# Kernel tuning notes

Measured on AMD Instinct MI355X. Metric: run time of the kernel, lower is better.

Reference implementation:

```python
import jax, jax.numpy as jnp
import numpy as np

B, T, D, NH, L = 8192, 100, 44, 64, 8  # batch, seq/ode steps, obs_dim, rnn hidden, latent


def setup_inputs() -> dict:
    key = jax.random.key(0)
    ks = jax.random.split(key, 12)
    s = 0.1
    return {
        "x": jax.random.normal(ks[0], (B, T, D), jnp.float32),
        "mask": jax.random.randint(ks[1], (B, T, D), 0, 2).astype(jnp.float32),
        "epsilon": jax.random.normal(ks[2], (B, L), jnp.float32),
        "Wi2h": jax.random.normal(ks[3], (D + NH, NH), jnp.float32) * s,
        "bi2h": jnp.zeros((NH,), jnp.float32),
        "Wh2o": jax.random.normal(ks[4], (NH, 2 * L), jnp.float32) * s,
        "bh2o": jnp.zeros((2 * L,), jnp.float32),
        "Wf1": jax.random.normal(ks[5], (L, NH), jnp.float32) * s,
        "bf1": jnp.zeros((NH,), jnp.float32),
        "Wf2": jax.random.normal(ks[6], (NH, NH), jnp.float32) * s,
        "bf2": jnp.zeros((NH,), jnp.float32),
        "Wf3": jax.random.normal(ks[7], (NH, L), jnp.float32) * s,
        "bf3": jnp.zeros((L,), jnp.float32),
        "Wd1": jax.random.normal(ks[8], (L, NH), jnp.float32) * s,
        "bd1": jnp.zeros((NH,), jnp.float32),
        "Wd2": jax.random.normal(ks[9], (NH, D), jnp.float32) * s,
        "bd2": jnp.zeros((D,), jnp.float32),
    }


def reference(x, mask, epsilon, Wi2h, bi2h, Wh2o, bh2o,
              Wf1, bf1, Wf2, bf2, Wf3, bf3, Wd1, bd1, Wd2, bd2):
    masked_x = x * mask  # [B,T,D]

    # --- reverse-time recognition RNN (scan over time, reversed) ---
    def rnn_step(h, obs):
        h = jnp.tanh(jnp.concatenate([obs, h], axis=1) @ Wi2h + bi2h)
        return h, None

    xs_rev = jnp.transpose(masked_x[:, ::-1, :], (1, 0, 2))  # [T,B,D]
    h0 = jnp.zeros((x.shape[0], Wi2h.shape[1]), x.dtype)
    h_final, _ = jax.lax.scan(rnn_step, h0, xs_rev)
    out = h_final @ Wh2o + bh2o  # [B,2L]
    qz0_mean, qz0_logvar = out[:, :L], out[:, L:]

    # reparameterized latent sample
    z0 = epsilon * jnp.exp(0.5 * qz0_logvar) + qz0_mean  # [B,L]

    # --- latent ODE dynamics, fixed-step RK4 over ts = linspace(0,1,100) ---
    def f(z):
        h1 = jax.nn.elu(z @ Wf1 + bf1)
        h2 = jax.nn.elu(h1 @ Wf2 + bf2)
        return h2 @ Wf3 + bf3

    dt = jnp.asarray(1.0 / (T - 1), x.dtype)

    def rk4_step(z, _):
        k1 = f(z)
        k2 = f(z + 0.5 * dt * k1)
        k3 = f(z + 0.5 * dt * k2)
        k4 = f(z + dt * k3)
        zn = z + (dt / 6.0) * (k1 + 2.0 * k2 + 2.0 * k3 + k4)
        return zn, zn

    _, zs = jax.lax.scan(rk4_step, z0, None, length=T - 1)  # [T-1,B,L]
    pred_z = jnp.transpose(jnp.concatenate([z0[None], zs], axis=0), (1, 0, 2))  # [B,T,L]

    # --- decoder ---
    pred_x = jax.nn.relu(pred_z @ Wd1 + bd1) @ Wd2 + bd2  # [B,T,D]

    # fill observed entries back in
    updated_x = jnp.where(masked_x != 0, masked_x, pred_x)

    # --- loss ---
    noise_logvar = 2.0 * jnp.log(jnp.asarray(0.3, x.dtype))
    log2pi = jnp.log(jnp.asarray(2.0 * np.pi, x.dtype))
    logpx = (-0.5 * (log2pi + noise_logvar +
                     (x - updated_x) ** 2 / jnp.exp(noise_logvar))).sum((-1, -2))  # [B]
    kl = (-0.5 * qz0_logvar + (jnp.exp(qz0_logvar) + qz0_mean ** 2) / 2.0 - 0.5).sum(-1)  # [B]
    loss = jnp.mean(-logpx + kl)
    return loss
```

## Files before the change

kernel.cpp:

```cpp
#include <hip/hip_runtime.h>
#include <stdint.h>


constexpr int B_ = 8192, T_ = 100, D_ = 44, NH_ = 64, L_ = 8;

typedef float f32x4 __attribute__((ext_vector_type(4)));
typedef uint32_t u32x2 __attribute__((ext_vector_type(2)));

#if __has_builtin(__builtin_amdgcn_mfma_f32_16x16x16bf16_1k)
typedef short frag16 __attribute__((ext_vector_type(4)));
#define MFMA16(a, b, c) __builtin_amdgcn_mfma_f32_16x16x16bf16_1k(a, b, c, 0, 0, 0)
#define USE_F16 0
#elif __has_builtin(__builtin_amdgcn_mfma_f32_16x16x16_bf16_1k)
typedef short frag16 __attribute__((ext_vector_type(4)));
#define MFMA16(a, b, c) __builtin_amdgcn_mfma_f32_16x16x16_bf16_1k(a, b, c, 0, 0, 0)
#define USE_F16 0
#elif __has_builtin(__builtin_amdgcn_mfma_f32_16x16x16_bf16)
typedef __bf16 frag16 __attribute__((ext_vector_type(4)));
#define MFMA16(a, b, c) __builtin_amdgcn_mfma_f32_16x16x16_bf16(a, b, c, 0, 0, 0)
#define USE_F16 0
#else
typedef _Float16 frag16 __attribute__((ext_vector_type(4)));
#define MFMA16(a, b, c) __builtin_amdgcn_mfma_f32_16x16x16f16(a, b, c, 0, 0, 0)
#define USE_F16 1
#endif

__device__ __forceinline__ float fexp2(float x) { return __builtin_amdgcn_exp2f(x); }
__device__ __forceinline__ float frcp(float x) { return __builtin_amdgcn_rcpf(x); }
__device__ __forceinline__ float fexp(float x) { return fexp2(x * 1.44269504088896341f); }
__device__ __forceinline__ float tanh_f(float x) {
  float e = fexp2(x * 2.88539008177792681f);
  return 1.0f - 2.0f * frcp(e + 1.0f);
}
__device__ __forceinline__ float elu_f(float x) { return x > 0.0f ? x : (fexp(x) - 1.0f); }

__device__ __forceinline__ uint32_t EW(float v) {
#if USE_F16
  return (uint32_t)__builtin_bit_cast(unsigned short, (_Float16)v);
#else
  return (uint32_t)__builtin_bit_cast(unsigned short, (__bf16)v);
#endif
}
__device__ __forceinline__ uint32_t PK2(float lo, float hi) { return EW(lo) | (EW(hi) << 16); }
__device__ __forceinline__ frag16 fr4(float a, float b, float c, float d) {
  u32x2 u = {PK2(a, b), PK2(c, d)};
  return __builtin_bit_cast(frag16, u);
}
__device__ __forceinline__ frag16 frpk(f32x4 v) {
  u32x2 u = {PK2(v[0], v[1]), PK2(v[2], v[3])};
  return __builtin_bit_cast(frag16, u);
}
__device__ __forceinline__ float f4get(const float4& f, int i) {
  return i == 0 ? f.x : (i == 1 ? f.y : (i == 2 ? f.z : f.w));
}

__global__ __launch_bounds__(64) void fused_kernel(
    const float* __restrict__ x, const float* __restrict__ mask,
    const float* __restrict__ eps,
    const float* __restrict__ Wi2h, const float* __restrict__ bi2h,
    const float* __restrict__ Wh2o, const float* __restrict__ bh2o,
    const float* __restrict__ Wf1, const float* __restrict__ bf1,
    const float* __restrict__ Wf2, const float* __restrict__ bf2,
    const float* __restrict__ Wf3, const float* __restrict__ bf3,
    const float* __restrict__ Wd1, const float* __restrict__ bd1,
    const float* __restrict__ Wd2, const float* __restrict__ bd2,
    float* __restrict__ part) {
  const int lane = threadIdx.x;
  const int c = lane & 15, q = lane >> 4;
  const int r0 = blockIdx.x * 16;
  const f32x4 fzero = {0.f, 0.f, 0.f, 0.f};
  const frag16 fgbias = fr4(1.0f, 0.f, 0.f, 0.f);

  frag16 Ai[4][7];
#pragma unroll
  for (int tau = 0; tau < 4; ++tau)
#pragma unroll
    for (int kc = 0; kc < 7; ++kc) {
      const int m = 16 * tau + c;
      float wv[4];
#pragma unroll
      for (int i = 0; i < 4; ++i) {
        const int k = 16 * kc + 4 * q + i;
        float v = 0.0f;
        if (k < 64) v = Wi2h[(44 + k) * 64 + m];
        else if (k < 108) v = Wi2h[(k - 64) * 64 + m];
        else if (k == 108) v = bi2h[m];
        wv[i] = v;
      }
      Ai[tau][kc] = fr4(wv[0], wv[1], wv[2], wv[3]);
    }
  frag16 Ah2o[4];
#pragma unroll
  for (int kc = 0; kc < 4; ++kc) {
    float wv[4];
#pragma unroll
    for (int i = 0; i < 4; ++i) wv[i] = Wh2o[(16 * kc + 4 * q + i) * 16 + c];
    Ah2o[kc] = fr4(wv[0], wv[1], wv[2], wv[3]);
  }
  f32x4 bo;
#pragma unroll
  for (int r = 0; r < 4; ++r) bo[r] = bh2o[4 * q + r];

  const float* xrowbase = x + (size_t)(r0 + c) * T_ * D_;
  const float* mrowbase = mask + (size_t)(r0 + c) * T_ * D_;

  auto load_obs = [&](int t, float4* xv, float4* mv) {
    const float* xp = xrowbase + (size_t)t * D_;
    const float* mp = mrowbase + (size_t)t * D_;
    xv[0] = *(const float4*)(xp + 4 * q);
    mv[0] = *(const float4*)(mp + 4 * q);
    xv[1] = *(const float4*)(xp + 16 + 4 * q);
    mv[1] = *(const float4*)(mp + 16 + 4 * q);
    float4 zz = {0.f, 0.f, 0.f, 0.f};
    xv[2] = zz; mv[2] = zz;
    if (q < 3) {
      xv[2] = *(const float4*)(xp + 32 + 4 * q);
      mv[2] = *(const float4*)(mp + 32 + 4 * q);
    }
  };

  f32x4 hc[4] = {};
  float4 xo[3], mo[3];
  load_obs(T_ - 1, xo, mo);

#pragma unroll 1
  for (int s = 0; s < T_; ++s) {
    const int t = T_ - 1 - s;
    float4 cx[3], cm[3];
#pragma unroll
    for (int j = 0; j < 3; ++j) { cx[j] = xo[j]; cm[j] = mo[j]; }
    if (t > 0) load_obs(t - 1, xo, mo);

    frag16 ob[3];
#pragma unroll
    for (int j = 0; j < 2; ++j) {
      u32x2 u = {PK2(cx[j].x * cm[j].x, cx[j].y * cm[j].y),
                 PK2(cx[j].z * cm[j].z, cx[j].w * cm[j].w)};
      ob[j] = __builtin_bit_cast(frag16, u);
    }
    {
      u32x2 u = {PK2(cx[2].x * cm[2].x, cx[2].y * cm[2].y),
                 PK2(cx[2].z * cm[2].z, cx[2].w * cm[2].w)};
      ob[2] = (q < 3) ? __builtin_bit_cast(frag16, u) : fgbias;
    }

    frag16 bh[4];
#pragma unroll
    for (int tau = 0; tau < 4; ++tau) bh[tau] = frpk(hc[tau]);

#pragma unroll
    for (int tau = 0; tau < 4; ++tau) {
      f32x4 aA = MFMA16(Ai[tau][0], bh[0], fzero);
      aA = MFMA16(Ai[tau][1], bh[1], aA);
      aA = MFMA16(Ai[tau][2], bh[2], aA);
      aA = MFMA16(Ai[tau][3], bh[3], aA);
      f32x4 aB = MFMA16(Ai[tau][4], ob[0], fzero);
      aB = MFMA16(Ai[tau][5], ob[1], aB);
      aB = MFMA16(Ai[tau][6], ob[2], aB);
#pragma unroll
      for (int r = 0; r < 4; ++r) hc[tau][r] = tanh_f(aA[r] + aB[r]);
    }
  }

  frag16 bhF[4];
#pragma unroll
  for (int tau = 0; tau < 4; ++tau) bhF[tau] = frpk(hc[tau]);
  f32x4 o = bo;
#pragma unroll
  for (int kc = 0; kc < 4; ++kc) o = MFMA16(Ah2o[kc], bhF[kc], o);

  float lv[4];
#pragma unroll
  for (int r = 0; r < 4; ++r)
    lv[r] = __int_as_float(__shfl(__float_as_int(o[r]), lane + 32, 64));

  float klt = 0.0f;
  f32x4 z = {};
  if (q < 2) {
    const float4 ev = *(const float4*)(eps + (size_t)(r0 + c) * 8 + 4 * q);
#pragma unroll
    for (int r = 0; r < 4; ++r) {
      const float m = o[r];
      z[r] = f4get(ev, r) * fexp(0.5f * lv[r]) + m;
      klt += -0.5f * lv[r] + (fexp(lv[r]) + m * m) * 0.5f - 0.5f;
    }
  }
  klt += __shfl_xor(klt, 1);  klt += __shfl_xor(klt, 2);
  klt += __shfl_xor(klt, 4);  klt += __shfl_xor(klt, 8);
  klt += __shfl_xor(klt, 16); klt += __shfl_xor(klt, 32);

  __builtin_amdgcn_sched_barrier(0);

  frag16 A1[4], A2[4][4], A3[4], Ad1[4], Ad2[3][4];
#pragma unroll
  for (int tau = 0; tau < 4; ++tau) {
    float w1[4], wd[4];
#pragma unroll
    for (int i = 0; i < 4; ++i) {
      const int k = 4 * q + i;
      w1[i] = k < 8 ? Wf1[k * 64 + 16 * tau + c] : (k == 8 ? bf1[16 * tau + c] : 0.0f);
      wd[i] = k < 8 ? Wd1[k * 64 + 16 * tau + c] : (k == 8 ? bd1[16 * tau + c] : 0.0f);
    }
    A1[tau] = fr4(w1[0], w1[1], w1[2], w1[3]);
    Ad1[tau] = fr4(wd[0], wd[1], wd[2], wd[3]);
  }
#pragma unroll
  for (int tau = 0; tau < 4; ++tau)
#pragma unroll
    for (int kc = 0; kc < 4; ++kc) {
      float wv[4];
#pragma unroll
      for (int i = 0; i < 4; ++i) wv[i] = Wf2[(16 * kc + 4 * q + i) * 64 + 16 * tau + c];
      A2[tau][kc] = fr4(wv[0], wv[1], wv[2], wv[3]);
    }
#pragma unroll
  for (int kc = 0; kc < 4; ++kc) {
    float wv[4];
#pragma unroll
    for (int i = 0; i < 4; ++i)
      wv[i] = (c < 8) ? Wf3[(16 * kc + 4 * q + i) * 8 + c] : 0.0f;
    A3[kc] = fr4(wv[0], wv[1], wv[2], wv[3]);
  }
#pragma unroll
  for (int tau = 0; tau < 3; ++tau)
#pragma unroll
    for (int kc = 0; kc < 4; ++kc) {
      const int m = 16 * tau + c;
      float wv[4];
#pragma unroll
      for (int i = 0; i < 4; ++i)
        wv[i] = (m < 44) ? Wd2[(16 * kc + 4 * q + i) * 44 + m] : 0.0f;
      Ad2[tau][kc] = fr4(wv[0], wv[1], wv[2], wv[3]);
    }
  f32x4 b2_[4], b3_, bd2_[3];
#pragma unroll
  for (int tau = 0; tau < 4; ++tau)
#pragma unroll
    for (int r = 0; r < 4; ++r) b2_[tau][r] = bf2[16 * tau + 4 * q + r];
#pragma unroll
  for (int r = 0; r < 4; ++r) b3_[r] = (q < 2) ? bf3[4 * q + r] : 0.0f;
#pragma unroll
  for (int tau = 0; tau < 3; ++tau)
#pragma unroll
    for (int r = 0; r < 4; ++r) {
      const int d = 16 * tau + 4 * q + r;
      bd2_[tau][r] = (d < 44) ? bd2[d] : 0.0f;
    }

  auto build_bz = [&](f32x4 zv) -> frag16 {
    u32x2 u = {PK2(zv[0], zv[1]), PK2(zv[2], zv[3])};
    if (q == 2) { u[0] = EW(1.0f); u[1] = 0u; }
    else if (q == 3) { u[0] = 0u; u[1] = 0u; }
    return __builtin_bit_cast(frag16, u);
  };

  auto feval = [&](frag16 bz) -> f32x4 {
    frag16 bh[4];
#pragma unroll
    for (int tau = 0; tau < 4; ++tau) {
      f32x4 h = MFMA16(A1[tau], bz, fzero);
#pragma unroll
      for (int r = 0; r < 4; ++r) h[r] = elu_f(h[r]);
      bh[tau] = frpk(h);
    }
    frag16 bg[4];
#pragma unroll
    for (int tau = 0; tau < 4; ++tau) {
      f32x4 g = b2_[tau];
#pragma unroll
      for (int kc = 0; kc < 4; ++kc) g = MFMA16(A2[tau][kc], bh[kc], g);
#pragma unroll
      for (int r = 0; r < 4; ++r) g[r] = elu_f(g[r]);
      bg[tau] = frpk(g);
    }
    f32x4 rr = b3_;
#pragma unroll
    for (int kc = 0; kc < 4; ++kc) rr = MFMA16(A3[kc], bg[kc], rr);
    return rr;
  };

  auto load_xm = [&](int t, float4* xv, float4* mv) {
#pragma unroll
    for (int tau = 0; tau < 3; ++tau) {
      const int d0 = 16 * tau + 4 * q;
      if (d0 < 44) {
        const size_t off = (size_t)(r0 + c) * T_ * D_ + (size_t)t * D_ + d0;
        xv[tau] = *(const float4*)(x + off);
        mv[tau] = *(const float4*)(mask + off);
      }
    }
  };

  const float dt = 1.0f / (float)(T_ - 1);
  const float hdt = 0.5f * dt;
  float qacc = 0.0f;

  float4 xc[3], mc[3], xn[3], mn[3];
  load_xm(0, xc, mc);

#pragma unroll 1
  for (int t = 0; t < T_; ++t) {
    if (t < T_ - 1) load_xm(t + 1, xn, mn);

    frag16 bz = build_bz(z);

    frag16 bhd[4];
#pragma unroll
    for (int tau = 0; tau < 4; ++tau) {
      f32x4 hd = MFMA16(Ad1[tau], bz, fzero);
#pragma unroll
      for (int r = 0; r < 4; ++r) hd[r] = fmaxf(hd[r], 0.0f);
      bhd[tau] = frpk(hd);
    }
#pragma unroll
    for (int tau = 0; tau < 3; ++tau) {
      f32x4 p = bd2_[tau];
#pragma unroll
      for (int kc = 0; kc < 4; ++kc) p = MFMA16(Ad2[tau][kc], bhd[kc], p);
      if (16 * tau + 4 * q < 44) {
#pragma unroll
        for (int r = 0; r < 4; ++r) {
          const float xa = f4get(xc[tau], r), ma = f4get(mc[tau], r);
          const float mx = xa * ma;
          const float upd = (mx != 0.0f) ? mx : p[r];
          const float df = xa - upd;
          qacc += df * df;
        }
      }
    }

    if (t < T_ - 1) {
      f32x4 k1 = feval(bz);
      f32x4 zt;
#pragma unroll
      for (int r = 0; r < 4; ++r) zt[r] = z[r] + hdt * k1[r];
      f32x4 k2 = feval(build_bz(zt));
#pragma unroll
      for (int r = 0; r < 4; ++r) zt[r] = z[r] + hdt * k2[r];
      f32x4 k3 = feval(build_bz(zt));
#pragma unroll
      for (int r = 0; r < 4; ++r) zt[r] = z[r] + dt * k3[r];
      f32x4 k4 = feval(build_bz(zt));
#pragma unroll
      for (int r = 0; r < 4; ++r)
        z[r] += (dt / 6.0f) * (k1[r] + 2.0f * (k2[r] + k3[r]) + k4[r]);
#pragma unroll
      for (int tau = 0; tau < 3; ++tau) { xc[tau] = xn[tau]; mc[tau] = mn[tau]; }
    }
  }

  float tot = qacc * (0.5f / 0.09f);
  tot += __shfl_xor(tot, 1);  tot += __shfl_xor(tot, 2);
  tot += __shfl_xor(tot, 4);  tot += __shfl_xor(tot, 8);
  tot += __shfl_xor(tot, 16); tot += __shfl_xor(tot, 32);
  if (lane == 0) part[blockIdx.x] = tot + klt;
}

__global__ __launch_bounds__(512) void reduce_kernel(const float* __restrict__ part,
                                                     float* __restrict__ out) {
  __shared__ float s[8];
  const int tid = threadIdx.x;
  float v = part[tid];
  v += __shfl_xor(v, 1);  v += __shfl_xor(v, 2);
  v += __shfl_xor(v, 4);  v += __shfl_xor(v, 8);
  v += __shfl_xor(v, 16); v += __shfl_xor(v, 32);
  if ((tid & 63) == 0) s[tid >> 6] = v;
  __syncthreads();
  if (tid == 0) {
    float acc = 0.0f;
#pragma unroll
    for (int i = 0; i < 8; ++i) acc += s[i];
    const float c0 = 0.28503427112126353f;
    out[0] = acc * (1.0f / (float)B_) - (float)(T_ * D_) * c0;
  }
}

extern "C" void kernel_launch(void* const* d_in, const int* in_sizes, int n_in,
                              void* d_out, int out_size, void* d_ws, size_t ws_size,
                              hipStream_t stream) {
  const float* x    = (const float*)d_in[0];
  const float* mask = (const float*)d_in[1];
  const float* eps  = (const float*)d_in[2];
  const float* Wi2h = (const float*)d_in[3];
  const float* bi2h = (const float*)d_in[4];
  const float* Wh2o = (const float*)d_in[5];
  const float* bh2o = (const float*)d_in[6];
  const float* Wf1  = (const float*)d_in[7];
  const float* bf1  = (const float*)d_in[8];
  const float* Wf2  = (const float*)d_in[9];
  const float* bf2  = (const float*)d_in[10];
  const float* Wf3  = (const float*)d_in[11];
  const float* bf3  = (const float*)d_in[12];
  const float* Wd1  = (const float*)d_in[13];
  const float* bd1  = (const float*)d_in[14];
  const float* Wd2  = (const float*)d_in[15];
  const float* bd2  = (const float*)d_in[16];

  float* loss = (float*)d_out;
  float* part = (float*)d_ws;

  fused_kernel<<<dim3(B_ / 16), dim3(64), 0, stream>>>(
      x, mask, eps, Wi2h, bi2h, Wh2o, bh2o, Wf1, bf1, Wf2, bf2, Wf3, bf3,
      Wd1, bd1, Wd2, bd2, part);
  reduce_kernel<<<dim3(1), dim3(512), 0, stream>>>(part, loss);
}
```

Before: 698.0 us.

## Split ODE integration and decoder into producer/consumer wavefronts via LDS ring

The block grows from one to two wavefronts. Wave 0 runs the recognition RNN and the RK4 integration, writing each step's latent state into an LDS ring and setting a per-step flag. Wave 1 spins on those flags, loads x and mask, and runs the decoder plus squared-error accumulation, so decoding overlaps with ODE stepping instead of running serially with it. The MFMA accumulation chains are also split into independent partial sums to shorten dependency latency. In exchange each block needs more threads and more LDS, and wave 1 busy-waits on the flags, which may lower occupancy.

Result: no change. 693.9 us (-0.6%).

```diff
diff --git a/kernel.cpp b/kernel.cpp
--- a/kernel.cpp
+++ b/kernel.cpp
@@ -54,7 +54,7 @@
   return i == 0 ? f.x : (i == 1 ? f.y : (i == 2 ? f.z : f.w));
 }
 
-__global__ __launch_bounds__(64) void fused_kernel(
+__global__ __launch_bounds__(128) void fused_kernel(
     const float* __restrict__ x, const float* __restrict__ mask,
     const float* __restrict__ eps,
     const float* __restrict__ Wi2h, const float* __restrict__ bi2h,
@@ -65,295 +65,344 @@
     const float* __restrict__ Wd1, const float* __restrict__ bd1,
     const float* __restrict__ Wd2, const float* __restrict__ bd2,
     float* __restrict__ part) {
-  const int lane = threadIdx.x;
+  const int tid = threadIdx.x;
+  const int wid = tid >> 6;
+  const int lane = tid & 63;
   const int c = lane & 15, q = lane >> 4;
   const int r0 = blockIdx.x * 16;
   const f32x4 fzero = {0.f, 0.f, 0.f, 0.f};
-  const frag16 fgbias = fr4(1.0f, 0.f, 0.f, 0.f);
-
-  frag16 Ai[4][7];
-#pragma unroll
-  for (int tau = 0; tau < 4; ++tau)
-#pragma unroll
-    for (int kc = 0; kc < 7; ++kc) {
-      const int m = 16 * tau + c;
-      float wv[4];
-#pragma unroll
-      for (int i = 0; i < 4; ++i) {
-        const int k = 16 * kc + 4 * q + i;
-        float v = 0.0f;
-        if (k < 64) v = Wi2h[(44 + k) * 64 + m];
-        else if (k < 108) v = Wi2h[(k - 64) * 64 + m];
-        else if (k == 108) v = bi2h[m];
-        wv[i] = v;
-      }
-      Ai[tau][kc] = fr4(wv[0], wv[1], wv[2], wv[3]);
-    }
-  frag16 Ah2o[4];
-#pragma unroll
-  for (int kc = 0; kc < 4; ++kc) {
-    float wv[4];
-#pragma unroll
-    for (int i = 0; i < 4; ++i) wv[i] = Wh2o[(16 * kc + 4 * q + i) * 16 + c];
-    Ah2o[kc] = fr4(wv[0], wv[1], wv[2], wv[3]);
-  }
-  f32x4 bo;
-#pragma unroll
-  for (int r = 0; r < 4; ++r) bo[r] = bh2o[4 * q + r];
-
-  const float* xrowbase = x + (size_t)(r0 + c) * T_ * D_;
-  const float* mrowbase = mask + (size_t)(r0 + c) * T_ * D_;
-
-  auto load_obs = [&](int t, float4* xv, float4* mv) {
-    const float* xp = xrowbase + (size_t)t * D_;
-    const float* mp = mrowbase + (size_t)t * D_;
-    xv[0] = *(const float4*)(xp + 4 * q);
-    mv[0] = *(const float4*)(mp + 4 * q);
-    xv[1] = *(const float4*)(xp + 16 + 4 * q);
-    mv[1] = *(const float4*)(mp + 16 + 4 * q);
-    float4 zz = {0.f, 0.f, 0.f, 0.f};
-    xv[2] = zz; mv[2] = zz;
-    if (q < 3) {
-      xv[2] = *(const float4*)(xp + 32 + 4 * q);
-      mv[2] = *(const float4*)(mp + 32 + 4 * q);
-    }
-  };
-
-  f32x4 hc[4] = {};
-  float4 xo[3], mo[3];
-  load_obs(T_ - 1, xo, mo);
-
-#pragma unroll 1
-  for (int s = 0; s < T_; ++s) {
-    const int t = T_ - 1 - s;
-    float4 cx[3], cm[3];
-#pragma unroll
-    for (int j = 0; j < 3; ++j) { cx[j] = xo[j]; cm[j] = mo[j]; }
-    if (t > 0) load_obs(t - 1, xo, mo);
-
-    frag16 ob[3];
-#pragma unroll
-    for (int j = 0; j < 2; ++j) {
-      u32x2 u = {PK2(cx[j].x * cm[j].x, cx[j].y * cm[j].y),
-                 PK2(cx[j].z * cm[j].z, cx[j].w * cm[j].w)};
-      ob[j] = __builtin_bit_cast(frag16, u);
-    }
-    {
-      u32x2 u = {PK2(cx[2].x * cm[2].x, cx[2].y * cm[2].y),
-                 PK2(cx[2].z * cm[2].z, cx[2].w * cm[2].w)};
-      ob[2] = (q < 3) ? __builtin_bit_cast(frag16, u) : fgbias;
-    }
-
-    frag16 bh[4];
-#pragma unroll
-    for (int tau = 0; tau < 4; ++tau) bh[tau] = frpk(hc[tau]);
-
-#pragma unroll
-    for (int tau = 0; tau < 4; ++tau) {
-      f32x4 aA = MFMA16(Ai[tau][0], bh[0], fzero);
-      aA = MFMA16(Ai[tau][1], bh[1], aA);
-      aA = MFMA16(Ai[tau][2], bh[2], aA);
-      aA = MFMA16(Ai[tau][3], bh[3], aA);
-      f32x4 aB = MFMA16(Ai[tau][4], ob[0], fzero);
-      aB = MFMA16(Ai[tau][5], ob[1], aB);
-      aB = MFMA16(Ai[tau][6], ob[2], aB);
-#pragma unroll
-      for (int r = 0; r < 4; ++r) hc[tau][r] = tanh_f(aA[r] + aB[r]);
-    }
-  }
-
-  frag16 bhF[4];
-#pragma unroll
-  for (int tau = 0; tau < 4; ++tau) bhF[tau] = frpk(hc[tau]);
-  f32x4 o = bo;
-#pragma unroll
-  for (int kc = 0; kc < 4; ++kc) o = MFMA16(Ah2o[kc], bhF[kc], o);
-
-  float lv[4];
-#pragma unroll
-  for (int r = 0; r < 4; ++r)
-    lv[r] = __int_as_float(__shfl(__float_as_int(o[r]), lane + 32, 64));
+
+  __shared__ __align__(16) uint32_t ring[6400];
+  __shared__ uint32_t flags[104];
+  __shared__ float sse_sh;
+
+  if (tid < 104) flags[tid] = 0u;
+  __syncthreads();
 
   float klt = 0.0f;
-  f32x4 z = {};
-  if (q < 2) {
-    const float4 ev = *(const float4*)(eps + (size_t)(r0 + c) * 8 + 4 * q);
-#pragma unroll
-    for (int r = 0; r < 4; ++r) {
-      const float m = o[r];
-      z[r] = f4get(ev, r) * fexp(0.5f * lv[r]) + m;
-      klt += -0.5f * lv[r] + (fexp(lv[r]) + m * m) * 0.5f - 0.5f;
-    }
-  }
-  klt += __shfl_xor(klt, 1);  klt += __shfl_xor(klt, 2);
-  klt += __shfl_xor(klt, 4);  klt += __shfl_xor(klt, 8);
-  klt += __shfl_xor(klt, 16); klt += __shfl_xor(klt, 32);
-
-  __builtin_amdgcn_sched_barrier(0);
-
-  frag16 A1[4], A2[4][4], A3[4], Ad1[4], Ad2[3][4];
-#pragma unroll
-  for (int tau = 0; tau < 4; ++tau) {
-    float w1[4], wd[4];
-#pragma unroll
-    for (int i = 0; i < 4; ++i) {
-      const int k = 4 * q + i;
-      w1[i] = k < 8 ? Wf1[k * 64 + 16 * tau + c] : (k == 8 ? bf1[16 * tau + c] : 0.0f);
-      wd[i] = k < 8 ? Wd1[k * 64 + 16 * tau + c] : (k == 8 ? bd1[16 * tau + c] : 0.0f);
-    }
-    A1[tau] = fr4(w1[0], w1[1], w1[2], w1[3]);
-    Ad1[tau] = fr4(wd[0], wd[1], wd[2], wd[3]);
-  }
-#pragma unroll
-  for (int tau = 0; tau < 4; ++tau)
+
+  if (wid == 0) {
+    const frag16 fgbias = fr4(1.0f, 0.f, 0.f, 0.f);
+
+    frag16 Ai[4][7];
+#pragma unroll
+    for (int tau = 0; tau < 4; ++tau)
+#pragma unroll
+      for (int kc = 0; kc < 7; ++kc) {
+        const int m = 16 * tau + c;
+        float wv[4];
+#pragma unroll
+        for (int i = 0; i < 4; ++i) {
+          const int k = 16 * kc + 4 * q + i;
+          float v = 0.0f;
+          if (k < 64) v = Wi2h[(44 + k) * 64 + m];
+          else if (k < 108) v = Wi2h[(k - 64) * 64 + m];
+          else if (k == 108) v = bi2h[m];
+          wv[i] = v;
+        }
+        Ai[tau][kc] = fr4(wv[0], wv[1], wv[2], wv[3]);
+      }
+    frag16 Ah2o[4];
 #pragma unroll
     for (int kc = 0; kc < 4; ++kc) {
       float wv[4];
 #pragma unroll
-      for (int i = 0; i < 4; ++i) wv[i] = Wf2[(16 * kc + 4 * q + i) * 64 + 16 * tau + c];
-      A2[tau][kc] = fr4(wv[0], wv[1], wv[2], wv[3]);
-    }
-#pragma unroll
-  for (int kc = 0; kc < 4; ++kc) {
-    float wv[4];
-#pragma unroll
-    for (int i = 0; i < 4; ++i)
-      wv[i] = (c < 8) ? Wf3[(16 * kc + 4 * q + i) * 8 + c] : 0.0f;
-    A3[kc] = fr4(wv[0], wv[1], wv[2], wv[3]);
+      for (int i = 0; i < 4; ++i) wv[i] = Wh2o[(16 * kc + 4 * q + i) * 16 + c];
+      Ah2o[kc] = fr4(wv[0], wv[1], wv[2], wv[3]);
+    }
+    f32x4 bo;
+#pragma unroll
+    for (int r = 0; r < 4; ++r) bo[r] = bh2o[4 * q + r];
+
+    const float* xrowbase = x + (size_t)(r0 + c) * T_ * D_;
+    const float* mrowbase = mask + (size_t)(r0 + c) * T_ * D_;
+
+    auto load_obs = [&](int t, float4* xv, float4* mv) {
+      const float* xp = xrowbase + (size_t)t * D_;
+      const float* mp = mrowbase + (size_t)t * D_;
+      xv[0] = *(const float4*)(xp + 4 * q);
+      mv[0] = *(const float4*)(mp + 4 * q);
+      xv[1] = *(const float4*)(xp + 16 + 4 * q);
+      mv[1] = *(const float4*)(mp + 16 + 4 * q);
+      float4 zz = {0.f, 0.f, 0.f, 0.f};
+      xv[2] = zz; mv[2] = zz;
+      if (q < 3) {
+        xv[2] = *(const float4*)(xp + 32 + 4 * q);
+        mv[2] = *(const float4*)(mp + 32 + 4 * q);
+      }
+    };
+
+    f32x4 hc[4] = {};
+    float4 xo[3], mo[3];
+    load_obs(T_ - 1, xo, mo);
+
+#pragma unroll 1
+    for (int s = 0; s < T_; ++s) {
+      const int t = T_ - 1 - s;
+      float4 cx[3], cm[3];
+#pragma unroll
+      for (int j = 0; j < 3; ++j) { cx[j] = xo[j]; cm[j] = mo[j]; }
+      if (t > 0) load_obs(t - 1, xo, mo);
+
+      frag16 ob[3];
+#pragma unroll
+      for (int j = 0; j < 2; ++j) {
+        u32x2 u = {PK2(cx[j].x * cm[j].x, cx[j].y * cm[j].y),
+                   PK2(cx[j].z * cm[j].z, cx[j].w * cm[j].w)};
+        ob[j] = __builtin_bit_cast(frag16, u);
+      }
+      {
+        u32x2 u = {PK2(cx[2].x * cm[2].x, cx[2].y * cm[2].y),
+                   PK2(cx[2].z * cm[2].z, cx[2].w * cm[2].w)};
+        ob[2] = (q < 3) ? __builtin_bit_cast(frag16, u) : fgbias;
+      }
+
+      frag16 bh[4];
+#pragma unroll
+      for (int tau = 0; tau < 4; ++tau) bh[tau] = frpk(hc[tau]);
+
+#pragma unroll
+      for (int tau = 0; tau < 4; ++tau) {
+        f32x4 pA = MFMA16(Ai[tau][0], bh[0], fzero);
+        pA = MFMA16(Ai[tau][1], bh[1], pA);
+        f32x4 pB = MFMA16(Ai[tau][2], bh[2], fzero);
+        pB = MFMA16(Ai[tau][3], bh[3], pB);
+        f32x4 pC = MFMA16(Ai[tau][4], ob[0], fzero);
+        pC = MFMA16(Ai[tau][5], ob[1], pC);
+        pC = MFMA16(Ai[tau][6], ob[2], pC);
+#pragma unroll
+        for (int r = 0; r < 4; ++r) hc[tau][r] = tanh_f(pA[r] + pB[r] + pC[r]);
+      }
+    }
+
+    frag16 bhF[4];
+#pragma unroll
+    for (int tau = 0; tau < 4; ++tau) bhF[tau] = frpk(hc[tau]);
+    f32x4 o = bo;
+#pragma unroll
+    for (int kc = 0; kc < 4; ++kc) o = MFMA16(Ah2o[kc], bhF[kc], o);
+
+    float lv[4];
+#pragma unroll
+    for (int r = 0; r < 4; ++r)
+      lv[r] = __int_as_float(__shfl(__float_as_int(o[r]), lane + 32, 64));
+
+    f32x4 z = {};
+    if (q < 2) {
+      const float4 ev = *(const float4*)(eps + (size_t)(r0 + c) * 8 + 4 * q);
+#pragma unroll
+      for (int r = 0; r < 4; ++r) {
+        const float m = o[r];
+        z[r] = f4get(ev, r) * fexp(0.5f * lv[r]) + m;
+        klt += -0.5f * lv[r] + (fexp(lv[r]) + m * m) * 0.5f - 0.5f;
+      }
+    }
+    klt += __shfl_xor(klt, 1);  klt += __shfl_xor(klt, 2);
+    klt += __shfl_xor(klt, 4);  klt += __shfl_xor(klt, 8);
+    klt += __shfl_xor(klt, 16); klt += __shfl_xor(klt, 32);
+
+    __builtin_amdgcn_sched_barrier(0);
+
+    frag16 A1[4], A2[4][4], A3[4];
+#pragma unroll
+    for (int tau = 0; tau < 4; ++tau) {
+      float w1[4];
+#pragma unroll
+      for (int i = 0; i < 4; ++i) {
+        const int k = 4 * q + i;
+        w1[i] = k < 8 ? Wf1[k * 64 + 16 * tau + c] : (k == 8 ? bf1[16 * tau + c] : 0.0f);
+      }
+      A1[tau] = fr4(w1[0], w1[1], w1[2], w1[3]);
+    }
+#pragma unroll
+    for (int tau = 0; tau < 4; ++tau)
+#pragma unroll
+      for (int kc = 0; kc < 4; ++kc) {
+        float wv[4];
+#pragma unroll
+        for (int i = 0; i < 4; ++i) wv[i] = Wf2[(16 * kc + 4 * q + i) * 64 + 16 * tau + c];
+        A2[tau][kc] = fr4(wv[0], wv[1], wv[2], wv[3]);
+      }
+#pragma unroll
+    for (int kc = 0; kc < 4; ++kc) {
+      float wv[4];
+#pragma unroll
+      for (int i = 0; i < 4; ++i)
+        wv[i] = (c < 8) ? Wf3[(16 * kc + 4 * q + i) * 8 + c] : 0.0f;
+      A3[kc] = fr4(wv[0], wv[1], wv[2], wv[3]);
+    }
+    f32x4 b2_[4], b3_;
+#pragma unroll
+    for (int tau = 0; tau < 4; ++tau)
+#pragma unroll
+      for (int r = 0; r < 4; ++r) b2_[tau][r] = bf2[16 * tau + 4 * q + r];
+#pragma unroll
+    for (int r = 0; r < 4; ++r) b3_[r] = (q < 2) ? bf3[4 * q + r] : 0.0f;
+
+    auto build_bz = [&](f32x4 zv) -> frag16 {
+      u32x2 u = {PK2(zv[0], zv[1]), PK2(zv[2], zv[3])};
+      if (q == 2) { u[0] = EW(1.0f); u[1] = 0u; }
+      else if (q == 3) { u[0] = 0u; u[1] = 0u; }
+      return __builtin_bit_cast(frag16, u);
+    };
+
+    auto feval = [&](frag16 bz) -> f32x4 {
+      frag16 bh[4];
+#pragma unroll
+      for (int tau = 0; tau < 4; ++tau) {
+        f32x4 h = MFMA16(A1[tau], bz, fzero);
+#pragma unroll
+        for (int r = 0; r < 4; ++r) h[r] = elu_f(h[r]);
+        bh[tau] = frpk(h);
+      }
+      frag16 bg[4];
+#pragma unroll
+      for (int tau = 0; tau < 4; ++tau) {
+        f32x4 ga = MFMA16(A2[tau][0], bh[0], b2_[tau]);
+        ga = MFMA16(A2[tau][1], bh[1], ga);
+        f32x4 gb = MFMA16(A2[tau][2], bh[2], fzero);
+        gb = MFMA16(A2[tau][3], bh[3], gb);
+#pragma unroll
+        for (int r = 0; r < 4; ++r) ga[r] = elu_f(ga[r] + gb[r]);
+        bg[tau] = frpk(ga);
+      }
+      f32x4 ra = MFMA16(A3[0], bg[0], b3_);
+      ra = MFMA16(A3[1], bg[1], ra);
+      f32x4 rb = MFMA16(A3[2], bg[2], fzero);
+      rb = MFMA16(A3[3], bg[3], rb);
+#pragma unroll
+      for (int r = 0; r < 4; ++r) ra[r] += rb[r];
+      return ra;
+    };
+
+    const float dt = 1.0f / (float)(T_ - 1);
+    const float hdt = 0.5f * dt;
+
+#pragma unroll 1
+    for (int t = 0; t < T_; ++t) {
+      if (q < 2) {
+        u32x2 v = {PK2(z[0], z[1]), PK2(z[2], z[3])};
+        *(u32x2*)(ring + (t * 32 + c * 2 + q) * 2) = v;
+      }
+      asm volatile("s_waitcnt lgkmcnt(0)" ::: "memory");
+      if (lane == 0) ((volatile uint32_t*)flags)[t] = 1u;
+
+      if (t < T_ - 1) {
+        f32x4 k1 = feval(build_bz(z));
+        f32x4 zt;
+#pragma unroll
+        for (int r = 0; r < 4; ++r) zt[r] = z[r] + hdt * k1[r];
+        f32x4 k2 = feval(build_bz(zt));
+#pragma unroll
+        for (int r = 0; r < 4; ++r) zt[r] = z[r] + hdt * k2[r];
+        f32x4 k3 = feval(build_bz(zt));
+#pragma unroll
+        for (int r = 0; r < 4; ++r) zt[r] = z[r] + dt * k3[r];
+        f32x4 k4 = feval(build_bz(zt));
+#pragma unroll
+        for (int r = 0; r < 4; ++r)
+          z[r] += (dt / 6.0f) * (k1[r] + 2.0f * (k2[r] + k3[r]) + k4[r]);
+      }
+    }
+  } else {
+    frag16 Ad1[4], Ad2[3][4];
+#pragma unroll
+    for (int tau = 0; tau < 4; ++tau) {
+      float wd[4];
+#pragma unroll
+      for (int i = 0; i < 4; ++i) {
+        const int k = 4 * q + i;
+        wd[i] = k < 8 ? Wd1[k * 64 + 16 * tau + c] : (k == 8 ? bd1[16 * tau + c] : 0.0f);
+      }
+      Ad1[tau] = fr4(wd[0], wd[1], wd[2], wd[3]);
+    }
+#pragma unroll
+    for (int tau = 0; tau < 3; ++tau)
+#pragma unroll
+      for (int kc = 0; kc < 4; ++kc) {
+        const int m = 16 * tau + c;
+        float wv[4];
+#pragma unroll
+        for (int i = 0; i < 4; ++i)
+          wv[i] = (m < 44) ? Wd2[(16 * kc + 4 * q + i) * 44 + m] : 0.0f;
+        Ad2[tau][kc] = fr4(wv[0], wv[1], wv[2], wv[3]);
+      }
+    f32x4 bd2_[3];
+#pragma unroll
+    for (int tau = 0; tau < 3; ++tau)
+#pragma unroll
+      for (int r = 0; r < 4; ++r) {
+        const int d = 16 * tau + 4 * q + r;
+        bd2_[tau][r] = (d < 44) ? bd2[d] : 0.0f;
+      }
+
+    float qacc = 0.0f;
+    volatile uint32_t* vf = flags;
+
+#pragma unroll 1
+    for (int t = 0; t < T_; ++t) {
+      float4 xc[3], mc[3];
+#pragma unroll
+      for (int tau = 0; tau < 3; ++tau) {
+        const int d0 = 16 * tau + 4 * q;
+        if (d0 < 44) {
+          const size_t off = (size_t)(r0 + c) * T_ * D_ + (size_t)t * D_ + d0;
+          xc[tau] = *(const float4*)(x + off);
+          mc[tau] = *(const float4*)(mask + off);
+        } else {
+          float4 zz = {0.f, 0.f, 0.f, 0.f};
+          xc[tau] = zz; mc[tau] = zz;
+        }
+      }
+
+      while (vf[t] == 0u) __builtin_amdgcn_s_sleep(1);
+      asm volatile("" ::: "memory");
+
+      frag16 bz;
+      {
+        u32x2 u = {0u, 0u};
+        if (q < 2) u = *(const u32x2*)(ring + (t * 32 + c * 2 + q) * 2);
+        else if (q == 2) u[0] = EW(1.0f);
+        bz = __builtin_bit_cast(frag16, u);
+      }
+
+      frag16 bhd[4];
+#pragma unroll
+      for (int tau = 0; tau < 4; ++tau) {
+        f32x4 hd = MFMA16(Ad1[tau], bz, fzero);
+#pragma unroll
+        for (int r = 0; r < 4; ++r) hd[r] = fmaxf(hd[r], 0.0f);
+        bhd[tau] = frpk(hd);
+      }
+#pragma unroll
+      for (int tau = 0; tau < 3; ++tau) {
+        f32x4 pa = MFMA16(Ad2[tau][0], bhd[0], bd2_[tau]);
+        pa = MFMA16(Ad2[tau][1], bhd[1], pa);
+        f32x4 pb = MFMA16(Ad2[tau][2], bhd[2], fzero);
+        pb = MFMA16(Ad2[tau][3], bhd[3], pb);
+        if (16 * tau + 4 * q < 44) {
+#pragma unroll
+          for (int r = 0; r < 4; ++r) {
+            const float p = pa[r] + pb[r];
+            const float xa = f4get(xc[tau], r), ma = f4get(mc[tau], r);
+            const float mx = xa * ma;
+            const float upd = (mx != 0.0f) ? mx : p;
+            const float df = xa - upd;
+            qacc += df * df;
+          }
+        }
+      }
+    }
+
+    float tot = qacc * (0.5f / 0.09f);
+    tot += __shfl_xor(tot, 1);  tot += __shfl_xor(tot, 2);
+    tot += __shfl_xor(tot, 4);  tot += __shfl_xor(tot, 8);
+    tot += __shfl_xor(tot, 16); tot += __shfl_xor(tot, 32);
+    if (lane == 0) sse_sh = tot;
   }
-#pragma unroll
-  for (int tau = 0; tau < 3; ++tau)
-#pragma unroll
-    for (int kc = 0; kc < 4; ++kc) {
-      const int m = 16 * tau + c;
-      float wv[4];
-#pragma unroll
-      for (int i = 0; i < 4; ++i)
-        wv[i] = (m < 44) ? Wd2[(16 * kc + 4 * q + i) * 44 + m] : 0.0f;
-      Ad2[tau][kc] = fr4(wv[0], wv[1], wv[2], wv[3]);
-    }
-  f32x4 b2_[4], b3_, bd2_[3];
-#pragma unroll
-  for (int tau = 0; tau < 4; ++tau)
-#pragma unroll
-    for (int r = 0; r < 4; ++r) b2_[tau][r] = bf2[16 * tau + 4 * q + r];
-#pragma unroll
-  for (int r = 0; r < 4; ++r) b3_[r] = (q < 2) ? bf3[4 * q + r] : 0.0f;
-#pragma unroll
-  for (int tau = 0; tau < 3; ++tau)
-#pragma unroll
-    for (int r = 0; r < 4; ++r) {
-      const int d = 16 * tau + 4 * q + r;
-      bd2_[tau][r] = (d < 44) ? bd2[d] : 0.0f;
-    }
-
-  auto build_bz = [&](f32x4 zv) -> frag16 {
-    u32x2 u = {PK2(zv[0], zv[1]), PK2(zv[2], zv[3])};
-    if (q == 2) { u[0] = EW(1.0f); u[1] = 0u; }
-    else if (q == 3) { u[0] = 0u; u[1] = 0u; }
-    return __builtin_bit_cast(frag16, u);
-  };
-
-  auto feval = [&](frag16 bz) -> f32x4 {
-    frag16 bh[4];
-#pragma unroll
-    for (int tau = 0; tau < 4; ++tau) {
-      f32x4 h = MFMA16(A1[tau], bz, fzero);
-#pragma unroll
-      for (int r = 0; r < 4; ++r) h[r] = elu_f(h[r]);
-      bh[tau] = frpk(h);
-    }
-    frag16 bg[4];
-#pragma unroll
-    for (int tau = 0; tau < 4; ++tau) {
-      f32x4 g = b2_[tau];
-#pragma unroll
-      for (int kc = 0; kc < 4; ++kc) g = MFMA16(A2[tau][kc], bh[kc], g);
-#pragma unroll
-      for (int r = 0; r < 4; ++r) g[r] = elu_f(g[r]);
-      bg[tau] = frpk(g);
-    }
-    f32x4 rr = b3_;
-#pragma unroll
-    for (int kc = 0; kc < 4; ++kc) rr = MFMA16(A3[kc], bg[kc], rr);
-    return rr;
-  };
-
-  auto load_xm = [&](int t, float4* xv, float4* mv) {
-#pragma unroll
-    for (int tau = 0; tau < 3; ++tau) {
-      const int d0 = 16 * tau + 4 * q;
-      if (d0 < 44) {
-        const size_t off = (size_t)(r0 + c) * T_ * D_ + (size_t)t * D_ + d0;
-        xv[tau] = *(const float4*)(x + off);
-        mv[tau] = *(const float4*)(mask + off);
-      }
-    }
-  };
-
-  const float dt = 1.0f / (float)(T_ - 1);
-  const float hdt = 0.5f * dt;
-  float qacc = 0.0f;
-
-  float4 xc[3], mc[3], xn[3], mn[3];
-  load_xm(0, xc, mc);
-
-#pragma unroll 1
-  for (int t = 0; t < T_; ++t) {
-    if (t < T_ - 1) load_xm(t + 1, xn, mn);
-
-    frag16 bz = build_bz(z);
-
-    frag16 bhd[4];
-#pragma unroll
-    for (int tau = 0; tau < 4; ++tau) {
-      f32x4 hd = MFMA16(Ad1[tau], bz, fzero);
-#pragma unroll
-      for (int r = 0; r < 4; ++r) hd[r] = fmaxf(hd[r], 0.0f);
-      bhd[tau] = frpk(hd);
-    }
-#pragma unroll
-    for (int tau = 0; tau < 3; ++tau) {
-      f32x4 p = bd2_[tau];
-#pragma unroll
-      for (int kc = 0; kc < 4; ++kc) p = MFMA16(Ad2[tau][kc], bhd[kc], p);
-      if (16 * tau + 4 * q < 44) {
-#pragma unroll
-        for (int r = 0; r < 4; ++r) {
-          const float xa = f4get(xc[tau], r), ma = f4get(mc[tau], r);
-          const float mx = xa * ma;
-          const float upd = (mx != 0.0f) ? mx : p[r];
-          const float df = xa - upd;
-          qacc += df * df;
-        }
-      }
-    }
-
-    if (t < T_ - 1) {
-      f32x4 k1 = feval(bz);
-      f32x4 zt;
-#pragma unroll
-      for (int r = 0; r < 4; ++r) zt[r] = z[r] + hdt * k1[r];
-      f32x4 k2 = feval(build_bz(zt));
-#pragma unroll
-      for (int r = 0; r < 4; ++r) zt[r] = z[r] + hdt * k2[r];
-      f32x4 k3 = feval(build_bz(zt));
-#pragma unroll
-      for (int r = 0; r < 4; ++r) zt[r] = z[r] + dt * k3[r];
-      f32x4 k4 = feval(build_bz(zt));
-#pragma unroll
-      for (int r = 0; r < 4; ++r)
-        z[r] += (dt / 6.0f) * (k1[r] + 2.0f * (k2[r] + k3[r]) + k4[r]);
-#pragma unroll
-      for (int tau = 0; tau < 3; ++tau) { xc[tau] = xn[tau]; mc[tau] = mn[tau]; }
-    }
-  }
-
-  float tot = qacc * (0.5f / 0.09f);
-  tot += __shfl_xor(tot, 1);  tot += __shfl_xor(tot, 2);
-  tot += __shfl_xor(tot, 4);  tot += __shfl_xor(tot, 8);
-  tot += __shfl_xor(tot, 16); tot += __shfl_xor(tot, 32);
-  if (lane == 0) part[blockIdx.x] = tot + klt;
+
+  __syncthreads();
+  if (tid == 0) part[blockIdx.x] = sse_sh + klt;
 }
 
 __global__ __launch_bounds__(512) void reduce_kernel(const float* __restrict__ part,
@@ -399,7 +448,7 @@
   float* loss = (float*)d_out;
   float* part = (float*)d_ws;
 
-  fused_kernel<<<dim3(B_ / 16), dim3(64), 0, stream>>>(
+  fused_kernel<<<dim3(B_ / 16), dim3(128), 0, stream>>>(
       x, mask, eps, Wi2h, bi2h, Wh2o, bh2o, Wf1, bf1, Wf2, bf2, Wf3, bf3,
       Wd1, bd1, Wd2, bd2, part);
   reduce_kernel<<<dim3(1), dim3(512), 0, stream>>>(part, loss);
```
